# Performance work log

Measured on AMD Instinct MI355X. Metric: run time of the kernel, lower is better.

## Reference

```python
import jax, jax.numpy as jnp
import numpy as np

N_DRUGS = 10000
N_REL = 500
N_TARGETS = 20000
DIM = 128
B = 8192
K = 64
MAX_SCALE = 2.5   # self.scale (non-trainable)
MARGIN = 8.0


def _lorentz_random(key, n, d, std):
    # mimic Lorentz.random_normal: gaussian spatial part, time = sqrt(1+||x||^2)
    x = jax.random.normal(key, (n, d), dtype=jnp.float32) * std
    nar = x[:, 1:]
    time = jnp.sqrt(1.0 + jnp.sum(nar * nar, axis=-1, keepdims=True))
    return jnp.concatenate([time, nar], axis=-1)


def setup_inputs() -> dict:
    key = jax.random.key(0)
    ks = jax.random.split(key, 6)
    std = 1.0 / np.sqrt(DIM)
    drug_entity = _lorentz_random(ks[0], N_DRUGS, DIM, std)
    target_entity = _lorentz_random(ks[1], N_TARGETS, DIM, std)
    relation_bias = jnp.zeros((N_REL, DIM), dtype=jnp.float32)
    # kaiming_uniform_ on [n_rel, dim, dim]: fan_in = dim*dim, bound = sqrt(6/fan_in)
    bound = np.sqrt(6.0 / (DIM * DIM))
    relation_transform = jax.random.uniform(ks[2], (N_REL, DIM, DIM), dtype=jnp.float32,
                                            minval=-bound, maxval=bound)
    bias_head = jnp.zeros((N_DRUGS,), dtype=jnp.float32)
    bias_tail = jnp.zeros((N_TARGETS,), dtype=jnp.float32)
    u_idx = jax.random.randint(ks[3], (B,), 0, N_DRUGS, dtype=jnp.int32)
    r_idx = jax.random.randint(ks[4], (B,), 0, N_REL, dtype=jnp.int32)
    v_idx = jax.random.randint(ks[5], (B, K), 0, N_TARGETS, dtype=jnp.int32)
    return {"u_idx": u_idx, "r_idx": r_idx, "v_idx": v_idx,
            "drug_entity": drug_entity, "target_entity": target_entity,
            "relation_bias": relation_bias, "relation_transform": relation_transform,
            "bias_head": bias_head, "bias_tail": bias_tail}


def reference(u_idx, r_idx, v_idx, drug_entity, target_entity,
              relation_bias, relation_transform, bias_head, bias_tail):
    head = drug_entity[u_idx]                # [B, d] gather
    W = relation_transform[r_idx]            # [B, d, d] gather
    rb = relation_bias[r_idx]                 # [B, d] gather
    # lorentz_linear4decoder: x = head @ W^T (per sample)
    x = jnp.einsum('bd,bed->be', head, W)     # [B, d]
    time = jax.nn.sigmoid(x[:, :1]) * MAX_SCALE + 1.1   # [B, 1], from pre-bias x
    x = x + rb                                 # bias added after time
    nar = x[:, 1:]                             # [B, d-1]
    nar = nar / jnp.sqrt(jnp.sum(nar * nar, axis=-1, keepdims=True) / (time * time - 1.0))
    tail = target_entity[v_idx]               # [B, K, d] gather
    # cinner: spatial dot minus time product
    cin = jnp.einsum('bd,bkd->bk', nar, tail[..., 1:]) - time * tail[..., 0]  # [B, K]
    neg_dist = MARGIN + 2.0 * cin
    return neg_dist + bias_head[u_idx][:, None] + bias_tail[v_idx]
```

## Files before the change

### kernel.cpp

```cpp
#include <hip/hip_runtime.h>
#include <math.h>

#define N_B 8192
#define N_K 64
#define DD  128

__global__ __launch_bounds__(256) void hybo_kernel(
    const int* __restrict__ u_idx, const int* __restrict__ r_idx,
    const int* __restrict__ v_idx, const float* __restrict__ drug_entity,
    const float* __restrict__ target_entity, const float* __restrict__ relation_bias,
    const float* __restrict__ relation_transform, const float* __restrict__ bias_head,
    const float* __restrict__ bias_tail, float* __restrict__ out)
{
    const int b    = blockIdx.x;
    const int tid  = threadIdx.x;
    const int lane = tid & 63;
    const int wave = tid >> 6;
    const int q    = lane & 15;
    const int g    = lane >> 4;

    __shared__ float x_lds[DD];
    __shared__ float y_lds[DD];
    __shared__ float red_lds[4];

    const int u = u_idx[b];
    const int r = r_idx[b];

    int vi[4];
#pragma unroll
    for (int i = 0; i < 4; ++i)
        vi[i] = v_idx[(size_t)b * N_K + wave * 16 + i * 4 + g];

    const float4 h0 = *reinterpret_cast<const float4*>(drug_entity + (size_t)u * DD + 8 * q);
    const float4 h1 = *reinterpret_cast<const float4*>(drug_entity + (size_t)u * DD + 8 * q + 4);

    const float* Wb = relation_transform + (size_t)r * DD * DD;
    float4 wv[16];
#pragma unroll
    for (int i = 0; i < 8; ++i) {
        const float* row = Wb + (wave * 32 + i * 4 + g) * DD + 8 * q;
        wv[2 * i]     = *reinterpret_cast<const float4*>(row);
        wv[2 * i + 1] = *reinterpret_cast<const float4*>(row + 4);
    }
#pragma unroll
    for (int i = 0; i < 8; ++i) {
        float p;
        p = wv[2 * i].x * h0.x;
        p = fmaf(wv[2 * i].y,     h0.y, p);
        p = fmaf(wv[2 * i].z,     h0.z, p);
        p = fmaf(wv[2 * i].w,     h0.w, p);
        p = fmaf(wv[2 * i + 1].x, h1.x, p);
        p = fmaf(wv[2 * i + 1].y, h1.y, p);
        p = fmaf(wv[2 * i + 1].z, h1.z, p);
        p = fmaf(wv[2 * i + 1].w, h1.w, p);
        p += __shfl_xor(p, 1, 64);
        p += __shfl_xor(p, 2, 64);
        p += __shfl_xor(p, 4, 64);
        p += __shfl_xor(p, 8, 64);
        if (q == 0) x_lds[wave * 32 + i * 4 + g] = p;
    }

    float4 t0[4], t1[4];
    float  bt[4];
#pragma unroll
    for (int i = 0; i < 4; ++i) {
        const float* trow = target_entity + (size_t)vi[i] * DD + 8 * q;
        t0[i] = *reinterpret_cast<const float4*>(trow);
        t1[i] = *reinterpret_cast<const float4*>(trow + 4);
        bt[i] = bias_tail[vi[i]];
    }

    __syncthreads();

    const float x0 = x_lds[0];
    float xv = 0.0f, sq = 0.0f;
    if (tid < DD) {
        xv = x_lds[tid] + relation_bias[(size_t)r * DD + tid];
        y_lds[tid] = xv;
        if (tid > 0) sq = xv * xv;
    }
    float ps = sq;
#pragma unroll
    for (int m = 32; m >= 1; m >>= 1) ps += __shfl_xor(ps, m, 64);
    if (lane == 0) red_lds[wave] = ps;
    __syncthreads();

    const float timev = 2.5f / (1.0f + expf(-x0)) + 1.1f;
    const float s = red_lds[0] + red_lds[1] + red_lds[2] + red_lds[3];
    const float f = sqrtf((timev * timev - 1.0f) / s);

    float4 ya = *reinterpret_cast<const float4*>(&y_lds[8 * q]);
    float4 yb = *reinterpret_cast<const float4*>(&y_lds[8 * q + 4]);
    ya.x = (q == 0) ? -timev : ya.x * f;
    ya.y *= f; ya.z *= f; ya.w *= f;
    yb.x *= f; yb.y *= f; yb.z *= f; yb.w *= f;

    const float bh = bias_head[u];

#pragma unroll
    for (int i = 0; i < 4; ++i) {
        float p;
        p = t0[i].x * ya.x;
        p = fmaf(t0[i].y, ya.y, p);
        p = fmaf(t0[i].z, ya.z, p);
        p = fmaf(t0[i].w, ya.w, p);
        p = fmaf(t1[i].x, yb.x, p);
        p = fmaf(t1[i].y, yb.y, p);
        p = fmaf(t1[i].z, yb.z, p);
        p = fmaf(t1[i].w, yb.w, p);
        p += __shfl_xor(p, 1, 64);
        p += __shfl_xor(p, 2, 64);
        p += __shfl_xor(p, 4, 64);
        p += __shfl_xor(p, 8, 64);
        if (q == 0)
            out[(size_t)b * N_K + wave * 16 + i * 4 + g] = fmaf(2.0f, p, 8.0f) + bh + bt[i];
    }
}

extern "C" void kernel_launch(void* const* d_in, const int* in_sizes, int n_in,
                              void* d_out, int out_size, void* d_ws, size_t ws_size,
                              hipStream_t stream) {
    const int*   u_idx  = (const int*)d_in[0];
    const int*   r_idx  = (const int*)d_in[1];
    const int*   v_idx  = (const int*)d_in[2];
    const float* drug   = (const float*)d_in[3];
    const float* targ   = (const float*)d_in[4];
    const float* rbias  = (const float*)d_in[5];
    const float* rtrans = (const float*)d_in[6];
    const float* bhead  = (const float*)d_in[7];
    const float* btail  = (const float*)d_in[8];
    float* out = (float*)d_out;

    hipLaunchKernelGGL(hybo_kernel, dim3(N_B), dim3(256), 0, stream,
                       u_idx, r_idx, v_idx, drug, targ, rbias, rtrans, bhead, btail, out);
}
```

Baseline: 195.3 us.

## Sort samples by relation and map relation classes to fixed XCDs for L2 reuse

Adds a single-block pre-pass that counting-sorts the batch by relation index. It builds a slot map so that each relation class (r mod 8) is assigned to block IDs with the same value mod 8, and therefore to the same XCD under round-robin block dispatch. The main kernel then processes samples grouped by relation, so the 64KB relation matrices can be reused from that XCD's L2 instead of being refetched for every sample. The cost is an extra serial sort launch, workspace traffic for the permutation arrays, and some idle early-exit blocks in a padded grid.

```diff
diff --git a/kernel.cpp b/kernel.cpp
--- a/kernel.cpp
+++ b/kernel.cpp
@@ -4,15 +4,88 @@
 #define N_B 8192
 #define N_K 64
 #define DD  128
-
-__global__ __launch_bounds__(256) void hybo_kernel(
-    const int* __restrict__ u_idx, const int* __restrict__ r_idx,
-    const int* __restrict__ v_idx, const float* __restrict__ drug_entity,
-    const float* __restrict__ target_entity, const float* __restrict__ relation_bias,
-    const float* __restrict__ relation_transform, const float* __restrict__ bias_head,
-    const float* __restrict__ bias_tail, float* __restrict__ out)
+#define N_RELC 500
+#define KMAX 1536
+
+__global__ __launch_bounds__(1024) void sort_kernel(const int* __restrict__ r_idx,
+                                                    const int* __restrict__ u_idx,
+                                                    int* __restrict__ perm,
+                                                    int* __restrict__ uperm,
+                                                    int* __restrict__ rperm,
+                                                    int* __restrict__ slotmap,
+                                                    int* __restrict__ cls_total)
 {
-    const int b    = blockIdx.x;
+    __shared__ int hist[512];
+    __shared__ int scan[512];
+    __shared__ int scan8[512];
+    __shared__ int cur[512];
+    const int t = threadIdx.x;
+    if (t < 512) hist[t] = 0;
+    __syncthreads();
+
+    int rv[8];
+#pragma unroll
+    for (int k = 0; k < 8; ++k) {
+        rv[k] = r_idx[t + 1024 * k];
+        atomicAdd(&hist[rv[k]], 1);
+    }
+    __syncthreads();
+    if (t < 512) { scan[t] = hist[t]; scan8[t] = hist[t]; }
+    __syncthreads();
+    for (int off = 1; off < 512; off <<= 1) {
+        int v = 0;
+        if (t < 512 && t >= off) v = scan[t - off];
+        __syncthreads();
+        if (t < 512) scan[t] += v;
+        __syncthreads();
+    }
+    for (int off = 8; off < 512; off <<= 1) {
+        int v = 0;
+        if (t < 512 && t >= off) v = scan8[t - off];
+        __syncthreads();
+        if (t < 512) scan8[t] += v;
+        __syncthreads();
+    }
+    if (t < 512) cur[t] = scan[t] - hist[t];
+    if (t < 8) {
+        const int last = t + 8 * ((N_RELC - 1 - t) >> 3);
+        cls_total[t] = scan8[last];
+    }
+    __syncthreads();
+#pragma unroll
+    for (int k = 0; k < 8; ++k) {
+        const int b   = t + 1024 * k;
+        const int r   = rv[k];
+        const int pos = atomicAdd(&cur[r], 1);
+        perm[pos]  = b;
+        uperm[pos] = u_idx[b];
+        rperm[pos] = r;
+        const int p    = pos - (scan[r] - hist[r]);
+        const int slot = (scan8[r] - hist[r]) + p;
+        slotmap[8 * slot + (r & 7)] = pos;
+    }
+}
+
+__global__ __launch_bounds__(256) void hybo_main(
+    const int* __restrict__ v_idx,
+    const float* __restrict__ drug_entity, const float* __restrict__ target_entity,
+    const float* __restrict__ relation_bias, const float* __restrict__ relation_transform,
+    const float* __restrict__ bias_head, const float* __restrict__ bias_tail,
+    const int* __restrict__ perm, const int* __restrict__ uperm,
+    const int* __restrict__ rperm, const int* __restrict__ slotmap,
+    const int* __restrict__ cls_total,
+    float* __restrict__ out)
+{
+    const int bid = blockIdx.x;
+    const int x   = bid & 7;
+    const int k   = bid >> 3;
+    if (k >= cls_total[x]) return;
+
+    const int pos = slotmap[bid];
+    const int b   = perm[pos];
+    const int u   = uperm[pos];
+    const int r   = rperm[pos];
+
     const int tid  = threadIdx.x;
     const int lane = tid & 63;
     const int wave = tid >> 6;
@@ -22,9 +95,6 @@
     __shared__ float x_lds[DD];
     __shared__ float y_lds[DD];
     __shared__ float red_lds[4];
-
-    const int u = u_idx[b];
-    const int r = r_idx[b];
 
     int vi[4];
 #pragma unroll
@@ -131,6 +201,15 @@
     const float* btail  = (const float*)d_in[8];
     float* out = (float*)d_out;
 
-    hipLaunchKernelGGL(hybo_kernel, dim3(N_B), dim3(256), 0, stream,
-                       u_idx, r_idx, v_idx, drug, targ, rbias, rtrans, bhead, btail, out);
+    int* perm     = (int*)d_ws;
+    int* uperm    = perm + N_B;
+    int* rperm    = uperm + N_B;
+    int* slotmap  = rperm + N_B;
+    int* cls      = slotmap + 8 * KMAX;
+
+    hipLaunchKernelGGL(sort_kernel, dim3(1), dim3(1024), 0, stream,
+                       r_idx, u_idx, perm, uperm, rperm, slotmap, cls);
+    hipLaunchKernelGGL(hybo_main, dim3(8 * KMAX), dim3(256), 0, stream,
+                       v_idx, drug, targ, rbias, rtrans, bhead, btail,
+                       perm, uperm, rperm, slotmap, cls, out);
 }
```

Result: faster. 173.7 us (-11.1%).
